# Performance work log

Hardware: AMD Instinct MI355X
Metric: run time of the kernel (lower is better)

Reference implementation:

```python
import jax, jax.numpy as jnp
import numpy as np

T = 8          # timesteps (init arg)
SCALE = 5.0    # surrogate gradient sharpness (init arg)

# Heaviside spike with sigmoid surrogate gradient (SurrogateSpike.apply equivalent)
@jax.custom_vjp
def spike_fn(mem, thr):
    return (mem >= thr).astype(mem.dtype)

def _spike_fwd(mem, thr):
    return spike_fn(mem, thr), mem - thr  # save delta for backward

def _spike_bwd(delta, g):
    sg = jax.nn.sigmoid(SCALE * delta)
    grad = g * sg * (1.0 - sg) * SCALE
    # threshold grad = -modified_grad, reduced to thr shape (1,)
    return grad, (-jnp.sum(grad)).reshape(1)

spike_fn.defvjp(_spike_fwd, _spike_bwd)


def setup_inputs() -> dict:
    key = jax.random.key(0)
    k1, _ = jax.random.split(key)
    TB, C, H, W = 256, 512, 16, 16  # T*B=256 (B=32)
    x = jax.random.uniform(k1, (TB, C, H, W), dtype=jnp.float32)
    thresh = jnp.array([2.0], dtype=jnp.float32)  # learnable scalar threshold
    return {"x": x, "thresh": thresh}


def reference(x, thresh):
    # ExpandTemporalDim: [T*B, ...] -> [T, B, ...]
    xs = x.reshape(T, x.shape[0] // T, *x.shape[1:])
    mem0 = 0.5 * thresh * jnp.ones_like(xs[0])  # mem init depends on thresh (grad flows)

    def step(mem, xt):
        m = mem + xt                      # integrate
        sb = spike_fn(m, thresh)          # fire (surrogate grad)
        sp = sb * thresh                  # spike scaled by threshold
        return m - sp, sp                 # soft reset

    _, spikes = jax.lax.scan(step, mem0, xs)  # [T, B, ...]
    # MergeTemporalDim: [T, B, ...] -> [T*B, ...]
    return spikes.reshape(x.shape)
```

## Files before the change

kernel.cpp:

```cpp
#include <hip/hip_runtime.h>


typedef float f4 __attribute__((ext_vector_type(4)));

constexpr int T_STEPS = 8;
constexpr int BLOCK   = 256;
constexpr int ILP     = 4;

__global__ __launch_bounds__(BLOCK, 2) void if_fwd_kernel(
    const f4* __restrict__ x,
    const float* __restrict__ thresh,
    f4* __restrict__ out,
    int stride4)
{
    const int i0 = blockIdx.x * (BLOCK * ILP) + threadIdx.x;

    const float thr = thresh[0];
    const float h   = 0.5f * thr;

    f4 xt[T_STEPS][ILP];
#pragma unroll
    for (int t = 0; t < T_STEPS; ++t) {
#pragma unroll
        for (int j = 0; j < ILP; ++j) {
            xt[t][j] = __builtin_nontemporal_load(
                x + (size_t)t * stride4 + i0 + j * BLOCK);
        }
    }
    __builtin_amdgcn_sched_barrier(0);

    f4 m[ILP];
#pragma unroll
    for (int j = 0; j < ILP; ++j) {
        m[j] = (f4){h, h, h, h};
    }

#pragma unroll
    for (int t = 0; t < T_STEPS; ++t) {
#pragma unroll
        for (int j = 0; j < ILP; ++j) {
            m[j] += xt[t][j];
            f4 s;
#pragma unroll
            for (int k = 0; k < 4; ++k) {
                s[k] = (m[j][k] >= thr) ? thr : 0.0f;
            }
            m[j] -= s;
            __builtin_nontemporal_store(
                s, out + (size_t)t * stride4 + i0 + j * BLOCK);
        }
    }
}

extern "C" void kernel_launch(void* const* d_in, const int* in_sizes, int n_in,
                              void* d_out, int out_size, void* d_ws, size_t ws_size,
                              hipStream_t stream) {
    const float* x      = (const float*)d_in[0];
    const float* thresh = (const float*)d_in[1];
    float* out          = (float*)d_out;

    const int total   = in_sizes[0];
    const int stride  = total / T_STEPS;
    const int stride4 = stride / 4;

    dim3 block(BLOCK);
    dim3 grid(stride4 / (BLOCK * ILP));
    if_fwd_kernel<<<grid, block, 0, stream>>>(
        (const f4*)x, thresh, (f4*)out, stride4);
}
```

Before: 217.3 us.

## Use persistent grid with double-buffered register prefetch across chunks

Replaces the one-chunk-per-block launch with a fixed grid of 256 blocks. Each block loops over its range and double-buffers register loads, so the next chunk's loads are in flight while the current chunk is computed and stored. ILP drops to 2 per buffer to keep register use in check. The aim is to hide memory latency and launch tail, at the cost of assuming sizes divide evenly and of fewer blocks to fill the GPU.

```diff
diff --git a/kernel.cpp b/kernel.cpp
--- a/kernel.cpp
+++ b/kernel.cpp
@@ -5,7 +5,9 @@
 
 constexpr int T_STEPS = 8;
 constexpr int BLOCK   = 256;
-constexpr int ILP     = 4;
+constexpr int ILP     = 2;
+constexpr int GRID    = 256;
+constexpr int CHUNK   = BLOCK * ILP;
 
 __global__ __launch_bounds__(BLOCK, 2) void if_fwd_kernel(
     const f4* __restrict__ x,
@@ -13,41 +15,67 @@
     f4* __restrict__ out,
     int stride4)
 {
-    const int i0 = blockIdx.x * (BLOCK * ILP) + threadIdx.x;
+    const int per_block = stride4 / GRID;
+    const int range0    = blockIdx.x * per_block;
+    const int niter     = per_block / CHUNK;
 
     const float thr = thresh[0];
     const float h   = 0.5f * thr;
 
-    f4 xt[T_STEPS][ILP];
+    f4 bufA[T_STEPS][ILP];
+    f4 bufB[T_STEPS][ILP];
+
+    auto issue = [&](f4 (&buf)[T_STEPS][ILP], int it) {
+        const int i0 = range0 + it * CHUNK + (int)threadIdx.x;
 #pragma unroll
-    for (int t = 0; t < T_STEPS; ++t) {
+        for (int t = 0; t < T_STEPS; ++t) {
+#pragma unroll
+            for (int j = 0; j < ILP; ++j) {
+                buf[t][j] = __builtin_nontemporal_load(
+                    x + (size_t)t * stride4 + i0 + j * BLOCK);
+            }
+        }
+    };
+
+    auto consume = [&](f4 (&buf)[T_STEPS][ILP], int it) {
+        const int i0 = range0 + it * CHUNK + (int)threadIdx.x;
+        f4 m[ILP];
 #pragma unroll
         for (int j = 0; j < ILP; ++j) {
-            xt[t][j] = __builtin_nontemporal_load(
-                x + (size_t)t * stride4 + i0 + j * BLOCK);
+            m[j] = (f4){h, h, h, h};
         }
-    }
+#pragma unroll
+        for (int t = 0; t < T_STEPS; ++t) {
+#pragma unroll
+            for (int j = 0; j < ILP; ++j) {
+                m[j] += buf[t][j];
+                f4 s;
+#pragma unroll
+                for (int k = 0; k < 4; ++k) {
+                    s[k] = (m[j][k] >= thr) ? thr : 0.0f;
+                }
+                m[j] -= s;
+                __builtin_nontemporal_store(
+                    s, out + (size_t)t * stride4 + i0 + j * BLOCK);
+            }
+        }
+    };
+
+    issue(bufA, 0);
+    __builtin_amdgcn_sched_barrier(0);
+    issue(bufB, 1);
     __builtin_amdgcn_sched_barrier(0);
 
-    f4 m[ILP];
-#pragma unroll
-    for (int j = 0; j < ILP; ++j) {
-        m[j] = (f4){h, h, h, h};
-    }
-
-#pragma unroll
-    for (int t = 0; t < T_STEPS; ++t) {
-#pragma unroll
-        for (int j = 0; j < ILP; ++j) {
-            m[j] += xt[t][j];
-            f4 s;
-#pragma unroll
-            for (int k = 0; k < 4; ++k) {
-                s[k] = (m[j][k] >= thr) ? thr : 0.0f;
-            }
-            m[j] -= s;
-            __builtin_nontemporal_store(
-                s, out + (size_t)t * stride4 + i0 + j * BLOCK);
+    for (int it = 0; it < niter; it += 2) {
+        consume(bufA, it);
+        if (it + 2 < niter) {
+            issue(bufA, it + 2);
+            __builtin_amdgcn_sched_barrier(0);
+        }
+        consume(bufB, it + 1);
+        if (it + 3 < niter) {
+            issue(bufB, it + 3);
+            __builtin_amdgcn_sched_barrier(0);
         }
     }
 }
@@ -64,7 +92,7 @@
     const int stride4 = stride / 4;
 
     dim3 block(BLOCK);
-    dim3 grid(stride4 / (BLOCK * ILP));
+    dim3 grid(GRID);
     if_fwd_kernel<<<grid, block, 0, stream>>>(
         (const f4*)x, thresh, (f4*)out, stride4);
 }
```

Result: slower. 226.2 us (+4.1%).
